# Kernel tuning notes

Measured on AMD Instinct MI355X. Metric: run time of the kernel, lower is better.

Reference implementation:

```python
import jax, jax.numpy as jnp
import numpy as np

N, E, G = 100000, 1600000, 1000
F_IN, H, C = 16, 64, 2
EPS = 1e-5


def setup_inputs() -> dict:
    key = jax.random.key(0)
    ks = jax.random.split(key, 8)

    def lin(k, i, o):
        return (jax.random.normal(k, (i, o), jnp.float32) / np.float32(np.sqrt(i)))

    return {
        "x": jax.random.normal(ks[0], (N, F_IN), jnp.float32),
        "edge_index": jax.random.randint(ks[1], (2, E), 0, N),
        "batch": jnp.sort(jax.random.randint(ks[2], (N,), 0, G)),
        # GraphNorm params: weight=1, bias=0, mean_scale(alpha)=1 (PyG init)
        "gn0_w": jnp.ones(F_IN, jnp.float32), "gn0_b": jnp.zeros(F_IN, jnp.float32), "gn0_a": jnp.ones(F_IN, jnp.float32),
        "W1": lin(ks[3], F_IN, H), "b1": jnp.zeros(H, jnp.float32),
        "gn1_w": jnp.ones(H, jnp.float32), "gn1_b": jnp.zeros(H, jnp.float32), "gn1_a": jnp.ones(H, jnp.float32),
        "W2": lin(ks[4], H, H), "b2": jnp.zeros(H, jnp.float32),
        "gn2_w": jnp.ones(H, jnp.float32), "gn2_b": jnp.zeros(H, jnp.float32), "gn2_a": jnp.ones(H, jnp.float32),
        "W3": lin(ks[5], H, H), "b3": jnp.zeros(H, jnp.float32),
        "Wd": lin(ks[6], H, H), "bd": jnp.zeros(H, jnp.float32),
        "Wo": lin(ks[7], H, C), "bo": jnp.zeros(C, jnp.float32),
    }


def _graph_norm(x, batch, w, b, a):
    counts = jnp.maximum(jax.ops.segment_sum(jnp.ones(x.shape[0], x.dtype), batch, G), 1.0)[:, None]
    mean = jax.ops.segment_sum(x, batch, G) / counts          # [G, F]
    out = x - a * mean[batch]
    var = jax.ops.segment_sum(out * out, batch, G) / counts   # [G, F]
    return w * (out * jax.lax.rsqrt(var + EPS)[batch]) + b


def _gcn_conv(x, W, b, src, dst):
    # PyG GCNConv: D^{-1/2}(A+I)D^{-1/2} X W + b, deg includes self-loop
    h = x @ W                                                  # [N, out]
    deg = jax.ops.segment_sum(jnp.ones(src.shape[0], x.dtype), dst, N) + 1.0
    dinv = jax.lax.rsqrt(deg)
    msg = h[src] * (dinv[src] * dinv[dst])[:, None]            # [E, out]
    agg = jax.ops.segment_sum(msg, dst, N) + h / deg[:, None]  # self-loop term: 1/deg
    return agg + b


def reference(x, edge_index, batch, gn0_w, gn0_b, gn0_a, W1, b1,
              gn1_w, gn1_b, gn1_a, W2, b2, gn2_w, gn2_b, gn2_a,
              W3, b3, Wd, bd, Wo, bo):
    src, dst = edge_index[0], edge_index[1]
    x = _graph_norm(x, batch, gn0_w, gn0_b, gn0_a)
    x = jax.nn.relu(_gcn_conv(x, W1, b1, src, dst))
    x = _graph_norm(x, batch, gn1_w, gn1_b, gn1_a)
    x = jax.nn.relu(_gcn_conv(x, W2, b2, src, dst))
    x = _graph_norm(x, batch, gn2_w, gn2_b, gn2_a)
    x = jax.nn.relu(_gcn_conv(x, W3, b3, src, dst))
    counts = jnp.maximum(jax.ops.segment_sum(jnp.ones(N, x.dtype), batch, G), 1.0)
    pooled = jax.ops.segment_sum(x, batch, G) / counts[:, None]  # global_mean_pool [G, H]
    # dropout p=0.5 is identity in eval mode
    h = jax.nn.relu(pooled @ Wd + bd)
    logits = h @ Wo + bo
    return jax.nn.softmax(logits, axis=1)
```

## Files before the change

kernel.cpp:

```cpp
#include <hip/hip_runtime.h>
#include <hip/hip_fp16.h>
#include <math.h>

#define NB_NODES 100000
#define NB_EDGES 1600000
#define NB_GRAPHS 1000
#define CAP 160
#define NBLK1 400
#define CHUNK 4000
#define NBUCK 391
#define BCAP 4608
constexpr float GN_EPS = 1e-5f;

__global__ __launch_bounds__(256) void k1_hist(const int* __restrict__ dst,
    int* __restrict__ hist, const int* __restrict__ batch, int* __restrict__ gstart) {
    __shared__ int h[NBUCK];
    int tid = threadIdx.x;
    for (int i = tid; i < NBUCK; i += 256) h[i] = 0;
    if (blockIdx.x < 4) {
        int g = blockIdx.x * 256 + tid;
        if (g <= NB_GRAPHS) {
            int lo = 0, hi = NB_NODES;
            while (lo < hi) {
                int mid = (lo + hi) >> 1;
                if (batch[mid] < g) lo = mid + 1; else hi = mid;
            }
            gstart[g] = lo;
        }
    }
    __syncthreads();
    int base = blockIdx.x * CHUNK;
    for (int i = tid; i < CHUNK; i += 256) atomicAdd(&h[dst[base + i] >> 8], 1);
    __syncthreads();
    for (int i = tid; i < NBUCK; i += 256) hist[blockIdx.x * NBUCK + i] = h[i];
}

__global__ __launch_bounds__(512) void k2a_scan(int* __restrict__ hist,
                                                int* __restrict__ total) {
    __shared__ int s[512];
    int b = blockIdx.x;
    int tid = threadIdx.x;
    int v = (tid < NBLK1) ? hist[tid * NBUCK + b] : 0;
    s[tid] = v;
    __syncthreads();
    for (int o = 1; o < 512; o <<= 1) {
        int t = (tid >= o) ? s[tid - o] : 0;
        __syncthreads();
        s[tid] += t;
        __syncthreads();
    }
    if (tid < NBLK1) hist[tid * NBUCK + b] = s[tid] - v;
    if (tid == 511) total[b] = s[511];
}

__global__ __launch_bounds__(256) void k3_scatter(const int* __restrict__ ei,
    const int* __restrict__ hist, const int* __restrict__ total,
    unsigned int* __restrict__ ebuf) {
    __shared__ int cur[NBUCK];
    __shared__ int sc[256];
    int tid = threadIdx.x;
    int e0 = 2 * tid, e1 = 2 * tid + 1;
    int v0 = (e0 < NBUCK) ? total[e0] : 0;
    int v1 = (e1 < NBUCK) ? total[e1] : 0;
    int own = v0 + v1;
    sc[tid] = own;
    __syncthreads();
    for (int o = 1; o < 256; o <<= 1) {
        int t = (tid >= o) ? sc[tid - o] : 0;
        __syncthreads();
        sc[tid] += t;
        __syncthreads();
    }
    int pre = sc[tid] - own;
    if (e0 < NBUCK) cur[e0] = pre + hist[blockIdx.x * NBUCK + e0];
    if (e1 < NBUCK) cur[e1] = pre + v0 + hist[blockIdx.x * NBUCK + e1];
    __syncthreads();
    int eb = blockIdx.x * CHUNK;
    for (int i = tid; i < CHUNK; i += 256) {
        int e = eb + i;
        int sidx = ei[e];
        int d = ei[NB_EDGES + e];
        int pos = atomicAdd(&cur[d >> 8], 1);
        ebuf[pos] = (unsigned int)sidx | ((unsigned int)(d & 255) << 24);
    }
}

__global__ __launch_bounds__(256) void k4_fine(const unsigned int* __restrict__ ebuf,
    const int* __restrict__ total, int* __restrict__ csr_src, int* __restrict__ rowptr,
    float* __restrict__ dinv) {
    __shared__ int arena[2 * BCAP + 768];
    unsigned int* epk = (unsigned int*)arena;
    int* outb  = arena + BCAP;
    int* cnt   = arena + 2 * BCAP;
    int* sbuf  = arena + 2 * BCAP + 256;
    int* cur2  = arena + 2 * BCAP + 512;
    int* bases = arena + 2 * BCAP;
    int b = blockIdx.x;
    int tid = threadIdx.x;
    int e0 = 2 * tid, e1 = 2 * tid + 1;
    int v0 = (e0 < NBUCK) ? total[e0] : 0;
    int v1 = (e1 < NBUCK) ? total[e1] : 0;
    int own = v0 + v1;
    cur2[tid] = own;
    __syncthreads();
    for (int o = 1; o < 256; o <<= 1) {
        int t = (tid >= o) ? cur2[tid - o] : 0;
        __syncthreads();
        cur2[tid] += t;
        __syncthreads();
    }
    int pre = cur2[tid] - own;
    if (e0 < NBUCK) bases[e0] = pre;
    if (e1 < NBUCK) bases[e1] = pre + v0;
    if (tid == 0) bases[NBUCK] = NB_EDGES;
    __syncthreads();
    int eb = bases[b], ee = bases[b + 1];
    __syncthreads();
    int m = ee - eb;
    if (m > BCAP) m = BCAP;
    for (int i = tid; i < m; i += 256) epk[i] = ebuf[eb + i];
    cnt[tid] = 0;
    __syncthreads();
    for (int i = tid; i < m; i += 256) atomicAdd(&cnt[epk[i] >> 24], 1);
    __syncthreads();
    int c = cnt[tid];
    sbuf[tid] = c;
    __syncthreads();
    for (int o = 1; o < 256; o <<= 1) {
        int t = (tid >= o) ? sbuf[tid - o] : 0;
        __syncthreads();
        sbuf[tid] += t;
        __syncthreads();
    }
    int off = sbuf[tid] - c;
    cur2[tid] = off;
    __syncthreads();
    for (int i = tid; i < m; i += 256) {
        unsigned int p = epk[i];
        int r = atomicAdd(&cur2[p >> 24], 1);
        outb[r] = (int)(p & 0x00FFFFFFu);
    }
    __syncthreads();
    for (int i = tid; i < m; i += 256) csr_src[eb + i] = outb[i];
    int node = b * 256 + tid;
    if (node < NB_NODES) {
        rowptr[node] = eb + off;
        dinv[node] = rsqrtf((float)(c + 1));
    }
    if (b == 0 && tid == 0) rowptr[NB_NODES] = NB_EDGES;
}

union HU {
    uint4 u;
    __half2 h[4];
};

__device__ __forceinline__ void pkacc(__half2* a, uint4 v) {
    HU x; x.u = v;
    a[0] = __hadd2(a[0], x.h[0]);
    a[1] = __hadd2(a[1], x.h[1]);
    a[2] = __hadd2(a[2], x.h[2]);
    a[3] = __hadd2(a[3], x.h[3]);
}

__device__ __forceinline__ __half2 shxor_h2(__half2 v, int m) {
    union { __half2 h; int i; } u;
    u.h = v;
    u.i = __shfl_xor(u.i, m, 64);
    return u.h;
}

__device__ __forceinline__ int agg4_core(const uint4* __restrict__ hsv,
    const int* __restrict__ rowptr, const int* __restrict__ csr_src,
    const float* __restrict__ dinv, const float* __restrict__ bias,
    int n0, int e, int lane, int f8, int e8, float r[8]) {
    int i2 = n0 + 2 < e ? n0 + 2 : e;
    int i3 = n0 + 3 < e ? n0 + 3 : e;
    int i4 = n0 + 4 < e ? n0 + 4 : e;
    int r0 = rowptr[n0], r1 = rowptr[n0 + 1], r2 = rowptr[i2];
    int r3 = rowptr[i3], r4 = rowptr[i4];
    int d0 = r1 - r0, d1 = r2 - r1, d2 = r3 - r2, d3 = r4 - r3;
    const uint4 Z = {0u, 0u, 0u, 0u};
    int idx0 = (lane < d0) ? csr_src[r0 + lane] : -1;
    int idx1 = (lane < d1) ? csr_src[r1 + lane] : -1;
    int idx2 = (lane < d2) ? csr_src[r2 + lane] : -1;
    int idx3 = (lane < d3) ? csr_src[r3 + lane] : -1;
    uint4 self = Z;
    if (e8 < 4 && n0 + e8 < e) self = hsv[(size_t)(n0 + e8) * 8 + f8];
    uint4 gA[8];
#pragma unroll
    for (int b = 0; b < 4; b++) {
        int u = __shfl(idx0, b * 8 + e8, 64);
        gA[b] = Z;
        if (u >= 0) gA[b] = hsv[(size_t)u * 8 + f8];
        int v = __shfl(idx1, b * 8 + e8, 64);
        gA[4 + b] = Z;
        if (v >= 0) gA[4 + b] = hsv[(size_t)v * 8 + f8];
    }
    uint4 gB[8];
#pragma unroll
    for (int b = 0; b < 4; b++) {
        int u = __shfl(idx2, b * 8 + e8, 64);
        gB[b] = Z;
        if (u >= 0) gB[b] = hsv[(size_t)u * 8 + f8];
        int v = __shfl(idx3, b * 8 + e8, 64);
        gB[4 + b] = Z;
        if (v >= 0) gB[4 + b] = hsv[(size_t)v * 8 + f8];
    }
    __half2 acc0[4], acc1[4], acc2[4], acc3[4];
    __half2 z2{__half(0.f), __half(0.f)};
    acc0[0] = acc0[1] = acc0[2] = acc0[3] = z2;
    acc1[0] = acc1[1] = acc1[2] = acc1[3] = z2;
    acc2[0] = acc2[1] = acc2[2] = acc2[3] = z2;
    acc3[0] = acc3[1] = acc3[2] = acc3[3] = z2;
    if (e8 == 0) pkacc(acc0, self);
    if (e8 == 1) pkacc(acc1, self);
    if (e8 == 2) pkacc(acc2, self);
    if (e8 == 3) pkacc(acc3, self);
#pragma unroll
    for (int b = 0; b < 4; b++) { pkacc(acc0, gA[b]); pkacc(acc1, gA[4 + b]); }
#pragma unroll
    for (int b = 0; b < 4; b++) { pkacc(acc2, gB[b]); pkacc(acc3, gB[4 + b]); }
    int tb0 = (d0 + 7) >> 3, tb1 = (d1 + 7) >> 3;
    int tb2 = (d2 + 7) >> 3, tb3 = (d3 + 7) >> 3;
    for (int b = 4; b < tb0 && b < 8; b++) {
        int u = __shfl(idx0, b * 8 + e8, 64);
        if (u >= 0) pkacc(acc0, hsv[(size_t)u * 8 + f8]);
    }
    for (int b = 4; b < tb1 && b < 8; b++) {
        int u = __shfl(idx1, b * 8 + e8, 64);
        if (u >= 0) pkacc(acc1, hsv[(size_t)u * 8 + f8]);
    }
    for (int b = 4; b < tb2 && b < 8; b++) {
        int u = __shfl(idx2, b * 8 + e8, 64);
        if (u >= 0) pkacc(acc2, hsv[(size_t)u * 8 + f8]);
    }
    for (int b = 4; b < tb3 && b < 8; b++) {
        int u = __shfl(idx3, b * 8 + e8, 64);
        if (u >= 0) pkacc(acc3, hsv[(size_t)u * 8 + f8]);
    }
    for (int b = 8; b < tb0; b++) {
        int j = r0 + b * 8 + e8;
        if (j < r1) pkacc(acc0, hsv[(size_t)csr_src[j] * 8 + f8]);
    }
    for (int b = 8; b < tb1; b++) {
        int j = r1 + b * 8 + e8;
        if (j < r2) pkacc(acc1, hsv[(size_t)csr_src[j] * 8 + f8]);
    }
    for (int b = 8; b < tb2; b++) {
        int j = r2 + b * 8 + e8;
        if (j < r3) pkacc(acc2, hsv[(size_t)csr_src[j] * 8 + f8]);
    }
    for (int b = 8; b < tb3; b++) {
        int j = r3 + b * 8 + e8;
        if (j < r4) pkacc(acc3, hsv[(size_t)csr_src[j] * 8 + f8]);
    }
#pragma unroll
    for (int c = 0; c < 4; c++) {
        __half2 t0 = acc0[c];
        t0 = __hadd2(t0, shxor_h2(t0, 8));
        t0 = __hadd2(t0, shxor_h2(t0, 16));
        t0 = __hadd2(t0, shxor_h2(t0, 32));
        acc0[c] = t0;
        __half2 t1 = acc1[c];
        t1 = __hadd2(t1, shxor_h2(t1, 8));
        t1 = __hadd2(t1, shxor_h2(t1, 16));
        t1 = __hadd2(t1, shxor_h2(t1, 32));
        acc1[c] = t1;
        __half2 t2 = acc2[c];
        t2 = __hadd2(t2, shxor_h2(t2, 8));
        t2 = __hadd2(t2, shxor_h2(t2, 16));
        t2 = __hadd2(t2, shxor_h2(t2, 32));
        acc2[c] = t2;
        __half2 t3 = acc3[c];
        t3 = __hadd2(t3, shxor_h2(t3, 8));
        t3 = __hadd2(t3, shxor_h2(t3, 16));
        t3 = __hadd2(t3, shxor_h2(t3, 32));
        acc3[c] = t3;
    }
    if (e8 >= 4) return -1;
    int node = n0 + e8;
    if (node >= e) return -1;
    const __half2* acc = (e8 == 0) ? acc0 : (e8 == 1) ? acc1 : (e8 == 2) ? acc2 : acc3;
    float dn = dinv[node];
    const float4* b4 = (const float4*)bias;
    float4 blo = b4[f8 * 2], bhi = b4[f8 * 2 + 1];
    float2 f0 = __half22float2(acc[0]);
    float2 f1 = __half22float2(acc[1]);
    float2 f2 = __half22float2(acc[2]);
    float2 f3 = __half22float2(acc[3]);
    r[0] = fmaf(f0.x, dn, blo.x); r[1] = fmaf(f0.y, dn, blo.y);
    r[2] = fmaf(f1.x, dn, blo.z); r[3] = fmaf(f1.y, dn, blo.w);
    r[4] = fmaf(f2.x, dn, bhi.x); r[5] = fmaf(f2.y, dn, bhi.y);
    r[6] = fmaf(f3.x, dn, bhi.z); r[7] = fmaf(f3.y, dn, bhi.w);
#pragma unroll
    for (int c = 0; c < 8; c++) r[c] = r[c] > 0.f ? r[c] : 0.f;
    return node;
}

__device__ __forceinline__ void aggnorm_body(__half* rows, int s, int cnt, int e,
    const uint4* __restrict__ hsv, const int* __restrict__ rowptr,
    const int* __restrict__ csr_src, const float* __restrict__ dinv,
    const float* __restrict__ bias, const float* __restrict__ gw,
    const float* __restrict__ gb, const float* __restrict__ ga,
    const float* __restrict__ W, __half* __restrict__ out,
    float* red, float* red2, float* sam, float* ssc, float* srow) {
    int tid = threadIdx.x, lane = tid & 63, wid = tid >> 6;
    int f8 = lane & 7, e8 = lane >> 3;
    int passes = (cnt + 15) >> 4;
    for (int p = 0; p < passes; ++p) {
        int n0 = __builtin_amdgcn_readfirstlane(s + p * 16 + wid * 4);
        if (n0 < e) {
            float r[8];
            int node = agg4_core(hsv, rowptr, csr_src, dinv, bias, n0, e, lane, f8, e8, r);
            if (node >= 0) {
                HU o;
                o.h[0] = __floats2half2_rn(r[0], r[1]);
                o.h[1] = __floats2half2_rn(r[2], r[3]);
                o.h[2] = __floats2half2_rn(r[4], r[5]);
                o.h[3] = __floats2half2_rn(r[6], r[7]);
                ((uint4*)rows)[(size_t)(node - s) * 8 + f8] = o.u;
            }
        }
    }
    __syncthreads();
    float cntf = (float)(cnt > 1 ? cnt : 1);
    float sum = 0.f, sq = 0.f;
    for (int i = wid; i < cnt; i += 4) {
        float v = __half2float(rows[(size_t)i * 64 + lane]);
        sum += v;
        sq = fmaf(v, v, sq);
    }
    red[tid] = sum; red2[tid] = sq;
    __syncthreads();
    for (int st = 2; st > 0; st >>= 1) {
        if (wid < st) { red[tid] += red[tid + st * 64]; red2[tid] += red2[tid + st * 64]; }
        __syncthreads();
    }
    if (tid < 64) {
        float m = red[tid] / cntf, q = red2[tid] / cntf;
        float am = ga[tid] * m;
        sam[tid] = am;
        ssc[tid] = gw[tid] * rsqrtf(q - 2.f * am * m + am * am + GN_EPS);
    }
    __syncthreads();
    float wcol[64];
#pragma unroll
    for (int k = 0; k < 64; k++) wcol[k] = W[k * 64 + lane];
    float am = sam[lane], sc = ssc[lane], bb = gb[lane];
    for (int i = wid; i < cnt; i += 4) {
        float nv = (__half2float(rows[(size_t)i * 64 + lane]) - am) * sc + bb;
        srow[wid * 64 + lane] = nv;
        float acc = 0.f;
#pragma unroll
        for (int k = 0; k < 64; k++) acc = fmaf(srow[wid * 64 + k], wcol[k], acc);
        out[(size_t)(s + i) * 64 + lane] = __float2half(acc * dinv[s + i]);
    }
}

__global__ __launch_bounds__(256, 4) void fused_aggnorm_k(
    const __half* __restrict__ hs_in, const int* __restrict__ gstart,
    const int* __restrict__ rowptr, const int* __restrict__ csr_src,
    const float* __restrict__ dinv, const float* __restrict__ bias,
    const float* __restrict__ gw, const float* __restrict__ gb,
    const float* __restrict__ ga, const float* __restrict__ W,
    __half* __restrict__ out, __half* __restrict__ spill) {
    __shared__ alignas(16) __half sA[CAP * 64];
    __shared__ float red[256], red2[256];
    __shared__ float sam[64], ssc[64];
    __shared__ float srow[4 * 64];
    int g = blockIdx.x;
    int s = gstart[g], e = gstart[g + 1], cnt = e - s;
    const uint4* hsv = (const uint4*)hs_in;
    if (cnt <= CAP)
        aggnorm_body(sA, s, cnt, e, hsv, rowptr, csr_src, dinv, bias,
                     gw, gb, ga, W, out, red, red2, sam, ssc, srow);
    else
        aggnorm_body(spill + (size_t)s * 64, s, cnt, e, hsv, rowptr, csr_src, dinv, bias,
                     gw, gb, ga, W, out, red, red2, sam, ssc, srow);
}

__global__ __launch_bounds__(256, 4) void fused_aggpool_k(
    const __half* __restrict__ hs_in, const int* __restrict__ gstart,
    const int* __restrict__ rowptr, const int* __restrict__ csr_src,
    const float* __restrict__ dinv, const float* __restrict__ bias,
    const float* __restrict__ Wd, const float* __restrict__ bd,
    const float* __restrict__ Wo, const float* __restrict__ bo,
    float* __restrict__ out) {
    __shared__ float wpart[4 * 64];
    __shared__ float sp[64];
    __shared__ float sh[64];
    __shared__ float sl[2];
    int tid = threadIdx.x, lane = tid & 63, wid = tid >> 6;
    int f8 = lane & 7, e8 = lane >> 3;
    int g = blockIdx.x;
    int s = gstart[g], e = gstart[g + 1], cnt = e - s;
    const uint4* hsv = (const uint4*)hs_in;
    float pacc[8];
#pragma unroll
    for (int j = 0; j < 8; j++) pacc[j] = 0.f;
    int passes = (cnt + 15) >> 4;
    for (int p = 0; p < passes; ++p) {
        int n0 = __builtin_amdgcn_readfirstlane(s + p * 16 + wid * 4);
        if (n0 < e) {
            float r[8];
            int node = agg4_core(hsv, rowptr, csr_src, dinv, bias, n0, e, lane, f8, e8, r);
            if (node >= 0) {
#pragma unroll
                for (int j = 0; j < 8; j++) pacc[j] += r[j];
            }
        }
    }
#pragma unroll
    for (int j = 0; j < 8; j++) {
        float v = pacc[j];
        v += __shfl_xor(v, 8, 64);
        v += __shfl_xor(v, 16, 64);
        v += __shfl_xor(v, 32, 64);
        pacc[j] = v;
    }
    if (lane < 8) {
#pragma unroll
        for (int j = 0; j < 8; j++) wpart[wid * 64 + lane * 8 + j] = pacc[j];
    }
    __syncthreads();
    float cntf = (float)(cnt > 1 ? cnt : 1);
    if (tid < 64)
        sp[tid] = (wpart[tid] + wpart[64 + tid] + wpart[128 + tid] + wpart[192 + tid]) / cntf;
    __syncthreads();
    if (tid < 64) {
        float acc = bd[tid];
        for (int k = 0; k < 64; k++) acc = fmaf(sp[k], Wd[k * 64 + tid], acc);
        sh[tid] = acc > 0.f ? acc : 0.f;
    }
    __syncthreads();
    if (tid < 2) {
        float l = bo[tid];
        for (int k = 0; k < 64; k++) l = fmaf(sh[k], Wo[k * 2 + tid], l);
        sl[tid] = l;
    }
    __syncthreads();
    if (tid < 2) {
        float m = fmaxf(sl[0], sl[1]);
        float e0 = expf(sl[0] - m), e1 = expf(sl[1] - m);
        out[g * 2 + tid] = (tid == 0 ? e0 : e1) / (e0 + e1);
    }
}

__device__ __forceinline__ void l1_gather(__half* rows16, int s, int cnt, int e,
    const uint4* __restrict__ yv, const int* __restrict__ rowptr,
    const int* __restrict__ csr_src, int tid) {
    int lane = tid & 63, wid = tid >> 6;
    int es = lane >> 1, f2 = lane & 1;
    uint4* r16 = (uint4*)rows16;
    const uint4 Z = {0u, 0u, 0u, 0u};
    __half2 z2{__half(0.f), __half(0.f)};
    int passes = (cnt + 15) >> 4;
    for (int p = 0; p < passes; ++p) {
        int lnb = p * 16 + wid * 4;
        int n0 = __builtin_amdgcn_readfirstlane(s + lnb);
        if (n0 >= e) continue;
        int i1 = n0 + 1 < e ? n0 + 1 : e;
        int i2 = n0 + 2 < e ? n0 + 2 : e;
        int i3 = n0 + 3 < e ? n0 + 3 : e;
        int i4 = n0 + 4 < e ? n0 + 4 : e;
        int r0 = rowptr[n0], r1 = rowptr[i1], r2 = rowptr[i2];
        int r3 = rowptr[i3], r4 = rowptr[i4];
        int d0 = r1 - r0, d1 = r2 - r1, d2 = r3 - r2, d3 = r4 - r3;
        int idx0 = (lane < d0) ? csr_src[r0 + lane] : -1;
        int idx1 = (lane < d1) ? csr_src[r1 + lane] : -1;
        int idx2 = (lane < d2) ? csr_src[r2 + lane] : -1;
        int idx3 = (lane < d3) ? csr_src[r3 + lane] : -1;
        uint4 self = Z;
        if (lane < 8 && lnb + (lane >> 1) < cnt)
            self = yv[(size_t)(s + lnb + (lane >> 1)) * 2 + f2];
        __half2 a0[4], a1[4], a2[4], a3[4];
        a0[0] = a0[1] = a0[2] = a0[3] = z2;
        a1[0] = a1[1] = a1[2] = a1[3] = z2;
        a2[0] = a2[1] = a2[2] = a2[3] = z2;
        a3[0] = a3[1] = a3[2] = a3[3] = z2;
        { int u = __shfl(idx0, es, 64); if (u >= 0) pkacc(a0, yv[(size_t)u * 2 + f2]); }
        { int u = __shfl(idx1, es, 64); if (u >= 0) pkacc(a1, yv[(size_t)u * 2 + f2]); }
        { int u = __shfl(idx2, es, 64); if (u >= 0) pkacc(a2, yv[(size_t)u * 2 + f2]); }
        { int u = __shfl(idx3, es, 64); if (u >= 0) pkacc(a3, yv[(size_t)u * 2 + f2]); }
        if (d0 > 32) { int u = __shfl(idx0, 32 + es, 64); if (u >= 0) pkacc(a0, yv[(size_t)u * 2 + f2]); }
        if (d1 > 32) { int u = __shfl(idx1, 32 + es, 64); if (u >= 0) pkacc(a1, yv[(size_t)u * 2 + f2]); }
        if (d2 > 32) { int u = __shfl(idx2, 32 + es, 64); if (u >= 0) pkacc(a2, yv[(size_t)u * 2 + f2]); }
        if (d3 > 32) { int u = __shfl(idx3, 32 + es, 64); if (u >= 0) pkacc(a3, yv[(size_t)u * 2 + f2]); }
        for (int b = 2; b * 32 < d0; ++b) { int t = b * 32 + es; if (t < d0) pkacc(a0, yv[(size_t)csr_src[r0 + t] * 2 + f2]); }
        for (int b = 2; b * 32 < d1; ++b) { int t = b * 32 + es; if (t < d1) pkacc(a1, yv[(size_t)csr_src[r1 + t] * 2 + f2]); }
        for (int b = 2; b * 32 < d2; ++b) { int t = b * 32 + es; if (t < d2) pkacc(a2, yv[(size_t)csr_src[r2 + t] * 2 + f2]); }
        for (int b = 2; b * 32 < d3; ++b) { int t = b * 32 + es; if (t < d3) pkacc(a3, yv[(size_t)csr_src[r3 + t] * 2 + f2]); }
#pragma unroll
        for (int j = 0; j < 4; ++j) {
            __half2 t;
            t = a0[j];
            t = __hadd2(t, shxor_h2(t, 2));
            t = __hadd2(t, shxor_h2(t, 4));
            t = __hadd2(t, shxor_h2(t, 8));
            t = __hadd2(t, shxor_h2(t, 16));
            t = __hadd2(t, shxor_h2(t, 32));
            a0[j] = t;
            t = a1[j];
            t = __hadd2(t, shxor_h2(t, 2));
            t = __hadd2(t, shxor_h2(t, 4));
            t = __hadd2(t, shxor_h2(t, 8));
            t = __hadd2(t, shxor_h2(t, 16));
            t = __hadd2(t, shxor_h2(t, 32));
            a1[j] = t;
            t = a2[j];
            t = __hadd2(t, shxor_h2(t, 2));
            t = __hadd2(t, shxor_h2(t, 4));
            t = __hadd2(t, shxor_h2(t, 8));
            t = __hadd2(t, shxor_h2(t, 16));
            t = __hadd2(t, shxor_h2(t, 32));
            a2[j] = t;
            t = a3[j];
            t = __hadd2(t, shxor_h2(t, 2));
            t = __hadd2(t, shxor_h2(t, 4));
            t = __hadd2(t, shxor_h2(t, 8));
            t = __hadd2(t, shxor_h2(t, 16));
            t = __hadd2(t, shxor_h2(t, 32));
            a3[j] = t;
        }
        if (lane < 8) {
            int k = lane >> 1;
            int ln = lnb + k;
            if (ln < cnt) {
                __half2 sel[4];
#pragma unroll
                for (int j = 0; j < 4; ++j)
                    sel[j] = (k == 0) ? a0[j] : (k == 1) ? a1[j] : (k == 2) ? a2[j] : a3[j];
                pkacc(sel, self);
                HU o;
                o.h[0] = sel[0]; o.h[1] = sel[1]; o.h[2] = sel[2]; o.h[3] = sel[3];
                r16[(size_t)ln * 2 + f2] = o.u;
            }
        }
    }
}

__device__ __forceinline__ void l1_body(__half* rows64, __half* rows16,
    int s, int cnt, int e,
    const uint4* __restrict__ yv, const int* __restrict__ rowptr,
    const int* __restrict__ csr_src, const float* __restrict__ dinv,
    const float* __restrict__ W1, const float* __restrict__ b1,
    const float* __restrict__ gw, const float* __restrict__ gb,
    const float* __restrict__ ga, const float* __restrict__ W2,
    __half* __restrict__ out,
    float* red, float* red2, float* sam, float* ssc, float* srow) {
    int tid = threadIdx.x, lane = tid & 63, wid = tid >> 6;
    l1_gather(rows16, s, cnt, e, yv, rowptr, csr_src, tid);
    __syncthreads();
    float w1c[16];
#pragma unroll
    for (int k = 0; k < 16; ++k) w1c[k] = W1[k * 64 + lane];
    float bb1 = b1[lane];
    const uint4* r16v = (const uint4*)rows16;
    float cntf = (float)(cnt > 1 ? cnt : 1);
    float sum = 0.f, sq = 0.f;
    for (int i = wid; i < cnt; i += 4) {
        HU q0, q1;
        q0.u = r16v[(size_t)i * 2];
        q1.u = r16v[(size_t)i * 2 + 1];
        float dn = dinv[s + i];
        float dot = 0.f;
#pragma unroll
        for (int j = 0; j < 4; ++j) {
            float2 v = __half22float2(q0.h[j]);
            dot = fmaf(v.x, w1c[2 * j], dot);
            dot = fmaf(v.y, w1c[2 * j + 1], dot);
        }
#pragma unroll
        for (int j = 0; j < 4; ++j) {
            float2 v = __half22float2(q1.h[j]);
            dot = fmaf(v.x, w1c[8 + 2 * j], dot);
            dot = fmaf(v.y, w1c[8 + 2 * j + 1], dot);
        }
        float h = fmaf(dot, dn, bb1);
        h = h > 0.f ? h : 0.f;
        rows64[(size_t)i * 64 + lane] = __float2half(h);
        sum += h;
        sq = fmaf(h, h, sq);
    }
    red[tid] = sum; red2[tid] = sq;
    __syncthreads();
    for (int st = 2; st > 0; st >>= 1) {
        if (wid < st) { red[tid] += red[tid + st * 64]; red2[tid] += red2[tid + st * 64]; }
        __syncthreads();
    }
    if (tid < 64) {
        float m = red[tid] / cntf, q = red2[tid] / cntf;
        float am = ga[tid] * m;
        sam[tid] = am;
        ssc[tid] = gw[tid] * rsqrtf(q - 2.f * am * m + am * am + GN_EPS);
    }
    __syncthreads();
    float wcol[64];
#pragma unroll
    for (int k = 0; k < 64; k++) wcol[k] = W2[k * 64 + lane];
    float am = sam[lane], sc = ssc[lane], bbg = gb[lane];
    for (int i = wid; i < cnt; i += 4) {
        float nv = (__half2float(rows64[(size_t)i * 64 + lane]) - am) * sc + bbg;
        srow[wid * 64 + lane] = nv;
        float acc = 0.f;
#pragma unroll
        for (int k = 0; k < 64; k++) acc = fmaf(srow[wid * 64 + k], wcol[k], acc);
        out[(size_t)(s + i) * 64 + lane] = __float2half(acc * dinv[s + i]);
    }
}

__global__ __launch_bounds__(256, 4) void fused_l1_k(
    const __half* __restrict__ y16, const int* __restrict__ gstart,
    const int* __restrict__ rowptr, const int* __restrict__ csr_src,
    const float* __restrict__ dinv, const float* __restrict__ W1,
    const float* __restrict__ b1, const float* __restrict__ gw,
    const float* __restrict__ gb, const float* __restrict__ ga,
    const float* __restrict__ W2, __half* __restrict__ out,
    __half* __restrict__ spill64, __half* __restrict__ spill16) {
    __shared__ alignas(16) __half sR64[CAP * 64];
    __shared__ alignas(16) __half sR16[CAP * 16];
    __shared__ float red[256], red2[256];
    __shared__ float sam[64], ssc[64];
    __shared__ float srow[4 * 64];
    int g = blockIdx.x;
    int s = gstart[g], e = gstart[g + 1], cnt = e - s;
    const uint4* yv = (const uint4*)y16;
    if (cnt <= CAP)
        l1_body(sR64, sR16, s, cnt, e, yv, rowptr, csr_src, dinv,
                W1, b1, gw, gb, ga, W2, out, red, red2, sam, ssc, srow);
    else
        l1_body(spill64 + (size_t)s * 64, spill16 + (size_t)s * 16, s, cnt, e,
                yv, rowptr, csr_src, dinv,
                W1, b1, gw, gb, ga, W2, out, red, red2, sam, ssc, srow);
}

__device__ __forceinline__ void l0_body(float* rows, int cnt, int s,
    const float* __restrict__ x, const float* __restrict__ gw,
    const float* __restrict__ gb, const float* __restrict__ ga,
    const float* __restrict__ dinv, __half* __restrict__ y16,
    float* red, float* red2, float* sstat, float* sscale, int tid) {
    int f = tid & 15, r = tid >> 4;
    float cntf = (float)(cnt > 1 ? cnt : 1);
    float sum = 0.f, sq = 0.f;
    for (int i = r; i < cnt; i += 32) {
        float v = x[(size_t)(s + i) * 16 + f];
        rows[i * 16 + f] = v;
        sum += v;
        sq = fmaf(v, v, sq);
    }
    red[tid] = sum; red2[tid] = sq;
    __syncthreads();
    for (int st = 16; st > 0; st >>= 1) {
        if (r < st) { red[tid] += red[tid + st * 16]; red2[tid] += red2[tid + st * 16]; }
        __syncthreads();
    }
    if (tid < 16) {
        float m = red[tid] / cntf, q = red2[tid] / cntf;
        float am = ga[tid] * m;
        sstat[tid] = am;
        sscale[tid] = gw[tid] * rsqrtf(q - 2.f * am * m + am * am + GN_EPS);
    }
    __syncthreads();
    float am = sstat[f], sc = sscale[f], bb = gb[f];
    for (int i = r; i < cnt; i += 32) {
        float nv = (rows[i * 16 + f] - am) * sc + bb;
        y16[(size_t)(s + i) * 16 + f] = __float2half(nv * dinv[s + i]);
    }
}

__global__ __launch_bounds__(512) void layer0_k(const float* __restrict__ x,
    const int* __restrict__ gstart, const float* __restrict__ gw,
    const float* __restrict__ gb, const float* __restrict__ ga,
    const float* __restrict__ dinv, __half* __restrict__ y16,
    float* __restrict__ spill16f) {
    __shared__ float sRows[CAP * 16];
    __shared__ float red[512], red2[512];
    __shared__ float sstat[16], sscale[16];
    int tid = threadIdx.x;
    int g = blockIdx.x;
    int s = gstart[g], e = gstart[g + 1], cnt = e - s;
    if (cnt <= CAP)
        l0_body(sRows, cnt, s, x, gw, gb, ga, dinv, y16, red, red2, sstat, sscale, tid);
    else
        l0_body(spill16f + (size_t)s * 16, cnt, s, x, gw, gb, ga, dinv, y16, red, red2, sstat, sscale, tid);
}

extern "C" void kernel_launch(void* const* d_in, const int* in_sizes, int n_in,
                              void* d_out, int out_size, void* d_ws, size_t ws_size,
                              hipStream_t stream) {
    const float* x    = (const float*)d_in[0];
    const int* ei     = (const int*)d_in[1];
    const int* batch  = (const int*)d_in[2];
    const float* gn0w = (const float*)d_in[3];
    const float* gn0b = (const float*)d_in[4];
    const float* gn0a = (const float*)d_in[5];
    const float* W1   = (const float*)d_in[6];
    const float* b1   = (const float*)d_in[7];
    const float* gn1w = (const float*)d_in[8];
    const float* gn1b = (const float*)d_in[9];
    const float* gn1a = (const float*)d_in[10];
    const float* W2   = (const float*)d_in[11];
    const float* b2   = (const float*)d_in[12];
    const float* gn2w = (const float*)d_in[13];
    const float* gn2b = (const float*)d_in[14];
    const float* gn2a = (const float*)d_in[15];
    const float* W3   = (const float*)d_in[16];
    const float* b3   = (const float*)d_in[17];
    const float* Wd   = (const float*)d_in[18];
    const float* bd   = (const float*)d_in[19];
    const float* Wo   = (const float*)d_in[20];
    const float* bo   = (const float*)d_in[21];

    char* p = (char*)d_ws;
    auto alloc = [&](size_t bytes) -> void* {
        void* r = (void*)p;
        p += (bytes + 255) & ~(size_t)255;
        return r;
    };
    __half* A        = (__half*)alloc((size_t)NB_NODES * 64 * 2);
    __half* B        = (__half*)alloc((size_t)NB_NODES * 64 * 2);
    __half* y16      = (__half*)alloc((size_t)NB_NODES * 16 * 2);
    int* rowptr      = (int*)alloc((size_t)(NB_NODES + 1) * 4);
    unsigned* ebuf   = (unsigned*)alloc((size_t)NB_EDGES * 4);
    int* csr_src     = (int*)alloc((size_t)NB_EDGES * 4);
    int* hist        = (int*)alloc((size_t)NBLK1 * NBUCK * 4);
    int* total       = (int*)alloc((size_t)NBUCK * 4);
    float* dinv      = (float*)alloc((size_t)NB_NODES * 4);
    int* gstart      = (int*)alloc((size_t)(NB_GRAPHS + 1) * 4);
    float* spill16f  = (float*)alloc((size_t)NB_NODES * 16 * 4);
    __half* spillH   = (__half*)alloc((size_t)NB_NODES * 64 * 2);
    __half* spillQ   = (__half*)alloc((size_t)NB_NODES * 16 * 2);

    k1_hist<<<NBLK1, 256, 0, stream>>>(ei + NB_EDGES, hist, batch, gstart);
    k2a_scan<<<NBUCK, 512, 0, stream>>>(hist, total);
    k3_scatter<<<NBLK1, 256, 0, stream>>>(ei, hist, total, ebuf);
    k4_fine<<<NBUCK, 256, 0, stream>>>(ebuf, total, csr_src, rowptr, dinv);

    layer0_k<<<NB_GRAPHS, 512, 0, stream>>>(x, gstart, gn0w, gn0b, gn0a, dinv, y16, spill16f);
    fused_l1_k<<<NB_GRAPHS, 256, 0, stream>>>(y16, gstart, rowptr, csr_src, dinv,
                                              W1, b1, gn1w, gn1b, gn1a, W2, A, spillH, spillQ);
    fused_aggnorm_k<<<NB_GRAPHS, 256, 0, stream>>>(A, gstart, rowptr, csr_src, dinv,
                                                   b2, gn2w, gn2b, gn2a, W3, B, spillH);
    fused_aggpool_k<<<NB_GRAPHS, 256, 0, stream>>>(B, gstart, rowptr, csr_src, dinv,
                                                   b3, Wd, bd, Wo, bo, (float*)d_out);
}
```

Baseline: 296.5 us.

## Stage graph edge indices in LDS and gather per node with thread pairs

Each block preloads its graph's CSR source indices into a shared-memory arena when they fit, then the layer-1 gather assigns one node to a pair of threads that accumulate neighbor rows serially with 4-way unrolling. This replaces the wave-per-4-nodes scheme that needed shuffles and cross-lane butterfly reductions. It cuts reduction overhead and global index loads. In exchange, per-thread serial latency is longer, load can be imbalanced on high-degree nodes, and the block uses more LDS.

```diff
diff --git a/kernel.cpp b/kernel.cpp
--- a/kernel.cpp
+++ b/kernel.cpp
@@ -6,6 +6,7 @@
 #define NB_EDGES 1600000
 #define NB_GRAPHS 1000
 #define CAP 160
+#define ECAP 2048
 #define NBLK1 400
 #define CHUNK 4000
 #define NBUCK 391
@@ -447,110 +448,57 @@
     }
 }
 
-__device__ __forceinline__ void l1_gather(__half* rows16, int s, int cnt, int e,
+__device__ __forceinline__ void l1_gather(__half* rows16, int s, int cnt,
     const uint4* __restrict__ yv, const int* __restrict__ rowptr,
-    const int* __restrict__ csr_src, int tid) {
-    int lane = tid & 63, wid = tid >> 6;
-    int es = lane >> 1, f2 = lane & 1;
+    const int* __restrict__ csr_src, const int* eidx, bool lds_e, int eb, int tid) {
+    int f2 = tid & 1;
     uint4* r16 = (uint4*)rows16;
-    const uint4 Z = {0u, 0u, 0u, 0u};
-    __half2 z2{__half(0.f), __half(0.f)};
-    int passes = (cnt + 15) >> 4;
-    for (int p = 0; p < passes; ++p) {
-        int lnb = p * 16 + wid * 4;
-        int n0 = __builtin_amdgcn_readfirstlane(s + lnb);
-        if (n0 >= e) continue;
-        int i1 = n0 + 1 < e ? n0 + 1 : e;
-        int i2 = n0 + 2 < e ? n0 + 2 : e;
-        int i3 = n0 + 3 < e ? n0 + 3 : e;
-        int i4 = n0 + 4 < e ? n0 + 4 : e;
-        int r0 = rowptr[n0], r1 = rowptr[i1], r2 = rowptr[i2];
-        int r3 = rowptr[i3], r4 = rowptr[i4];
-        int d0 = r1 - r0, d1 = r2 - r1, d2 = r3 - r2, d3 = r4 - r3;
-        int idx0 = (lane < d0) ? csr_src[r0 + lane] : -1;
-        int idx1 = (lane < d1) ? csr_src[r1 + lane] : -1;
-        int idx2 = (lane < d2) ? csr_src[r2 + lane] : -1;
-        int idx3 = (lane < d3) ? csr_src[r3 + lane] : -1;
-        uint4 self = Z;
-        if (lane < 8 && lnb + (lane >> 1) < cnt)
-            self = yv[(size_t)(s + lnb + (lane >> 1)) * 2 + f2];
-        __half2 a0[4], a1[4], a2[4], a3[4];
-        a0[0] = a0[1] = a0[2] = a0[3] = z2;
-        a1[0] = a1[1] = a1[2] = a1[3] = z2;
-        a2[0] = a2[1] = a2[2] = a2[3] = z2;
-        a3[0] = a3[1] = a3[2] = a3[3] = z2;
-        { int u = __shfl(idx0, es, 64); if (u >= 0) pkacc(a0, yv[(size_t)u * 2 + f2]); }
-        { int u = __shfl(idx1, es, 64); if (u >= 0) pkacc(a1, yv[(size_t)u * 2 + f2]); }
-        { int u = __shfl(idx2, es, 64); if (u >= 0) pkacc(a2, yv[(size_t)u * 2 + f2]); }
-        { int u = __shfl(idx3, es, 64); if (u >= 0) pkacc(a3, yv[(size_t)u * 2 + f2]); }
-        if (d0 > 32) { int u = __shfl(idx0, 32 + es, 64); if (u >= 0) pkacc(a0, yv[(size_t)u * 2 + f2]); }
-        if (d1 > 32) { int u = __shfl(idx1, 32 + es, 64); if (u >= 0) pkacc(a1, yv[(size_t)u * 2 + f2]); }
-        if (d2 > 32) { int u = __shfl(idx2, 32 + es, 64); if (u >= 0) pkacc(a2, yv[(size_t)u * 2 + f2]); }
-        if (d3 > 32) { int u = __shfl(idx3, 32 + es, 64); if (u >= 0) pkacc(a3, yv[(size_t)u * 2 + f2]); }
-        for (int b = 2; b * 32 < d0; ++b) { int t = b * 32 + es; if (t < d0) pkacc(a0, yv[(size_t)csr_src[r0 + t] * 2 + f2]); }
-        for (int b = 2; b * 32 < d1; ++b) { int t = b * 32 + es; if (t < d1) pkacc(a1, yv[(size_t)csr_src[r1 + t] * 2 + f2]); }
-        for (int b = 2; b * 32 < d2; ++b) { int t = b * 32 + es; if (t < d2) pkacc(a2, yv[(size_t)csr_src[r2 + t] * 2 + f2]); }
-        for (int b = 2; b * 32 < d3; ++b) { int t = b * 32 + es; if (t < d3) pkacc(a3, yv[(size_t)csr_src[r3 + t] * 2 + f2]); }
-#pragma unroll
-        for (int j = 0; j < 4; ++j) {
-            __half2 t;
-            t = a0[j];
-            t = __hadd2(t, shxor_h2(t, 2));
-            t = __hadd2(t, shxor_h2(t, 4));
-            t = __hadd2(t, shxor_h2(t, 8));
-            t = __hadd2(t, shxor_h2(t, 16));
-            t = __hadd2(t, shxor_h2(t, 32));
-            a0[j] = t;
-            t = a1[j];
-            t = __hadd2(t, shxor_h2(t, 2));
-            t = __hadd2(t, shxor_h2(t, 4));
-            t = __hadd2(t, shxor_h2(t, 8));
-            t = __hadd2(t, shxor_h2(t, 16));
-            t = __hadd2(t, shxor_h2(t, 32));
-            a1[j] = t;
-            t = a2[j];
-            t = __hadd2(t, shxor_h2(t, 2));
-            t = __hadd2(t, shxor_h2(t, 4));
-            t = __hadd2(t, shxor_h2(t, 8));
-            t = __hadd2(t, shxor_h2(t, 16));
-            t = __hadd2(t, shxor_h2(t, 32));
-            a2[j] = t;
-            t = a3[j];
-            t = __hadd2(t, shxor_h2(t, 2));
-            t = __hadd2(t, shxor_h2(t, 4));
-            t = __hadd2(t, shxor_h2(t, 8));
-            t = __hadd2(t, shxor_h2(t, 16));
-            t = __hadd2(t, shxor_h2(t, 32));
-            a3[j] = t;
-        }
-        if (lane < 8) {
-            int k = lane >> 1;
-            int ln = lnb + k;
-            if (ln < cnt) {
-                __half2 sel[4];
-#pragma unroll
-                for (int j = 0; j < 4; ++j)
-                    sel[j] = (k == 0) ? a0[j] : (k == 1) ? a1[j] : (k == 2) ? a2[j] : a3[j];
-                pkacc(sel, self);
-                HU o;
-                o.h[0] = sel[0]; o.h[1] = sel[1]; o.h[2] = sel[2]; o.h[3] = sel[3];
-                r16[(size_t)ln * 2 + f2] = o.u;
+    for (int ln = (tid >> 1); ln < cnt; ln += 128) {
+        int rb = rowptr[s + ln];
+        int d = rowptr[s + ln + 1] - rb;
+        HU acc;
+        acc.u = yv[(size_t)(s + ln) * 2 + f2];
+        if (lds_e) {
+            int o = rb - eb;
+            int t = 0;
+            for (; t + 4 <= d; t += 4) {
+                int u0 = eidx[o + t], u1 = eidx[o + t + 1];
+                int u2 = eidx[o + t + 2], u3 = eidx[o + t + 3];
+                uint4 g0 = yv[(size_t)u0 * 2 + f2];
+                uint4 g1 = yv[(size_t)u1 * 2 + f2];
+                uint4 g2 = yv[(size_t)u2 * 2 + f2];
+                uint4 g3 = yv[(size_t)u3 * 2 + f2];
+                pkacc(acc.h, g0);
+                pkacc(acc.h, g1);
+                pkacc(acc.h, g2);
+                pkacc(acc.h, g3);
+            }
+            for (; t < d; ++t) {
+                int u = eidx[o + t];
+                pkacc(acc.h, yv[(size_t)u * 2 + f2]);
+            }
+        } else {
+            for (int t = 0; t < d; ++t) {
+                int u = csr_src[rb + t];
+                pkacc(acc.h, yv[(size_t)u * 2 + f2]);
             }
         }
+        r16[(size_t)ln * 2 + f2] = acc.u;
     }
 }
 
 __device__ __forceinline__ void l1_body(__half* rows64, __half* rows16,
-    int s, int cnt, int e,
+    int s, int cnt,
     const uint4* __restrict__ yv, const int* __restrict__ rowptr,
-    const int* __restrict__ csr_src, const float* __restrict__ dinv,
+    const int* __restrict__ csr_src, const int* eidx, bool lds_e, int eb,
+    const float* __restrict__ dinv,
     const float* __restrict__ W1, const float* __restrict__ b1,
     const float* __restrict__ gw, const float* __restrict__ gb,
     const float* __restrict__ ga, const float* __restrict__ W2,
     __half* __restrict__ out,
     float* red, float* red2, float* sam, float* ssc, float* srow) {
     int tid = threadIdx.x, lane = tid & 63, wid = tid >> 6;
-    l1_gather(rows16, s, cnt, e, yv, rowptr, csr_src, tid);
+    l1_gather(rows16, s, cnt, yv, rowptr, csr_src, eidx, lds_e, eb, tid);
     __syncthreads();
     float w1c[16];
 #pragma unroll
@@ -620,18 +568,24 @@
     __half* __restrict__ spill64, __half* __restrict__ spill16) {
     __shared__ alignas(16) __half sR64[CAP * 64];
     __shared__ alignas(16) __half sR16[CAP * 16];
+    __shared__ int arena[ECAP];
     __shared__ float red[256], red2[256];
     __shared__ float sam[64], ssc[64];
     __shared__ float srow[4 * 64];
+    int tid = threadIdx.x;
     int g = blockIdx.x;
     int s = gstart[g], e = gstart[g + 1], cnt = e - s;
+    int eb = rowptr[s], m = rowptr[e] - eb;
     const uint4* yv = (const uint4*)y16;
+    bool lds_e = (m <= ECAP);
+    if (lds_e) for (int i = tid; i < m; i += 256) arena[i] = csr_src[eb + i];
+    __syncthreads();
     if (cnt <= CAP)
-        l1_body(sR64, sR16, s, cnt, e, yv, rowptr, csr_src, dinv,
+        l1_body(sR64, sR16, s, cnt, yv, rowptr, csr_src, arena, lds_e, eb, dinv,
                 W1, b1, gw, gb, ga, W2, out, red, red2, sam, ssc, srow);
     else
-        l1_body(spill64 + (size_t)s * 64, spill16 + (size_t)s * 16, s, cnt, e,
-                yv, rowptr, csr_src, dinv,
+        l1_body(spill64 + (size_t)s * 64, spill16 + (size_t)s * 16, s, cnt,
+                yv, rowptr, csr_src, arena, lds_e, eb, dinv,
                 W1, b1, gw, gb, ga, W2, out, red, red2, sam, ssc, srow);
 }
 
```

Result: faster. 277.4 us (median of 2 runs) (-6.4%).
